# Kernel tuning notes

Measured on AMD Instinct MI355X. Metric: run time of the kernel, lower is better.

## Reference

```python
import jax, jax.numpy as jnp
import numpy as np

B, N, D = 256, 512, 512
H = 512            # step_context_dim
HEADS = 8
KEY = H // HEADS
T = 128            # number of decode steps
TANH_CLIP = 10.0
TEMP = 1.0
VEHICLE_CAP = 1.0
BATTERY_CAP = 1.0
NEG = -1e9         # stands in for -inf; safe under softmax/vjp


def setup_inputs() -> dict:
    key = jax.random.key(0)
    ks = jax.random.split(key, 10)
    embedding = jax.random.normal(ks[0], (B, N, D), dtype=jnp.float32)
    current_nodes = jax.random.randint(ks[1], (B, T), 0, N)
    used_capacity = jax.random.uniform(ks[2], (B, T), dtype=jnp.float32)
    used_battery = jax.random.uniform(ks[3], (B, T), dtype=jnp.float32)
    current_time = jax.random.uniform(ks[4], (B, T), dtype=jnp.float32)
    mask = jax.random.randint(ks[5], (B, T, N), 0, 2).astype(bool)
    mask = mask.at[:, :, 0].set(False)  # ensure at least one feasible node
    s = 0.02
    W_context = jax.random.normal(ks[6], (D, H), dtype=jnp.float32) * s
    W_kvlogit = jax.random.normal(ks[7], (D, 3 * H), dtype=jnp.float32) * s
    W_step = jax.random.normal(ks[8], (D + 3, H), dtype=jnp.float32) * s
    W_out = jax.random.normal(ks[9], (H, H), dtype=jnp.float32) * s
    return {"embedding": embedding, "current_nodes": current_nodes,
            "used_capacity": used_capacity, "used_battery": used_battery,
            "current_time": current_time, "mask": mask,
            "W_context": W_context, "W_kvlogit": W_kvlogit,
            "W_step": W_step, "W_out": W_out}


def reference(embedding, current_nodes, used_capacity, used_battery,
              current_time, mask, W_context, W_kvlogit, W_step, W_out):
    b, n, d = embedding.shape
    t = current_nodes.shape[1]
    # fixed context from mean graph embedding: [B,1,H]
    fixed_context = jnp.einsum('bd,dh->bh', embedding.mean(axis=1), W_context)[:, None, :]
    # shared K/V/logit-K projections: [B,N,3H]
    kvl = jnp.einsum('bnd,de->bne', embedding, W_kvlogit)
    glimpse_K, glimpse_V, logit_K = jnp.split(kvl, 3, axis=-1)
    glimpse_K = glimpse_K.reshape(b, n, HEADS, KEY).transpose(0, 2, 1, 3)  # [B,h,N,k]
    glimpse_V = glimpse_V.reshape(b, n, HEADS, KEY).transpose(0, 2, 1, 3)  # [B,h,N,k]
    # per-step context: gathered current-node embedding + 3 scalar state features
    cur_emb = jnp.take_along_axis(
        embedding, current_nodes[:, :, None], axis=1)  # [B,T,D]
    next_nodes = jnp.concatenate(
        [cur_emb,
         (VEHICLE_CAP - used_capacity)[..., None],
         (BATTERY_CAP - used_battery)[..., None],
         current_time[..., None]], axis=-1)            # [B,T,D+3]
    query = fixed_context + jnp.einsum('btd,dh->bth', next_nodes, W_step)  # [B,T,H]
    # multi-head single-query glimpse attention over all T steps at once
    Q = query.reshape(b, t, HEADS, KEY)
    compat = jnp.einsum('bthk,bhnk->bhtn', Q, glimpse_K) / np.sqrt(KEY)
    compat = jnp.where(mask[:, None, :, :], NEG, compat)
    attn = jax.nn.softmax(compat, axis=-1)
    heads_out = jnp.einsum('bhtn,bhnk->bthk', attn, glimpse_V).reshape(b, t, H)
    glimpse = jnp.einsum('bth,ho->bto', heads_out, W_out)  # project_out
    logits = jnp.einsum('bth,bnh->btn', glimpse, logit_K) / np.sqrt(H)
    logits = jnp.tanh(logits) * TANH_CLIP
    logits = jnp.where(mask, NEG, logits)
    log_p = jax.nn.log_softmax(logits / TEMP, axis=-1)  # [B,T,N]
    return log_p
```

## Files before the change

kernel.cpp:

```cpp
#include <hip/hip_runtime.h>
#include <hip/hip_bf16.h>
#include <hip/hip_fp8.h>
#include <stdint.h>

typedef unsigned char  u8;
typedef unsigned short u16;
typedef unsigned int   u32;
typedef unsigned long long u64;
typedef __attribute__((ext_vector_type(4))) float f32x4;
typedef __attribute__((ext_vector_type(8))) short s16x8;

#define NEG_INF (-1e9f)

__device__ __forceinline__ u16 f2bf(float f) {
  __hip_bfloat16 h = __float2bfloat16(f);
  return __builtin_bit_cast(u16, h);
}

__device__ __forceinline__ u8 f2fp8(float f) {
  __hip_fp8_e4m3 h(f);
  return (u8)h.__x;
}

__device__ __forceinline__ f32x4 mfma16(s16x8 a, s16x8 b, f32x4 c) {
  return __builtin_amdgcn_mfma_f32_16x16x32_bf16(a, b, c, 0, 0, 0);
}

__device__ __forceinline__ f32x4 mfma8(long a, long b, f32x4 c) {
  return __builtin_amdgcn_mfma_f32_16x16x32_fp8_fp8(a, b, c, 0, 0, 0);
}

#define GLOAD16(g, l)                                                        \
  __builtin_amdgcn_global_load_lds(                                          \
      (const __attribute__((address_space(1))) unsigned int*)(g),            \
      (__attribute__((address_space(3))) unsigned int*)(l), 16, 0, 0)
#define GLOAD4(g, l)                                                         \
  __builtin_amdgcn_global_load_lds(                                          \
      (const __attribute__((address_space(1))) unsigned int*)(g),            \
      (__attribute__((address_space(3))) unsigned int*)(l), 4, 0, 0)

#define WAITV(n) asm volatile("s_waitcnt vmcnt(" #n ")" ::: "memory")
#define WAITLGKM asm volatile("s_waitcnt lgkmcnt(0)" ::: "memory")
#define SBAR __builtin_amdgcn_sched_barrier(0)
#define HBAR __builtin_amdgcn_s_barrier()

__global__ void detect_mask_kernel(const u32* __restrict__ mraw, u32* __restrict__ flag) {
  __shared__ int any;
  if (threadIdx.x == 0) any = 0;
  __syncthreads();
  int loc = 0;
  for (int i = threadIdx.x; i < 16384; i += 256) {
    u32 v = mraw[i];
    if (v & 0xFFFFFF00u) loc = 1;
  }
  if (loc) atomicOr(&any, 1);
  __syncthreads();
  if (threadIdx.x == 0) *flag = any ? 1u : 4u;
}

__global__ __launch_bounds__(256) void maskprep_kernel(const void* __restrict__ mraw,
                                                       const u32* __restrict__ flag,
                                                       unsigned char* __restrict__ mb) {
  long long idx = (long long)blockIdx.x * 256 + threadIdx.x;
  long long bt = idx >> 6;
  int ch = (int)(idx & 63);
  unsigned char byte = 0;
  if (*flag == 1) {
    u64 v = *(const u64*)((const unsigned char*)mraw + bt * 512 + ch * 8);
#pragma unroll
    for (int i = 0; i < 8; i++)
      if ((v >> (8 * i)) & 0xFFull) byte |= (unsigned char)(1 << i);
  } else {
    const int* p = (const int*)mraw + bt * 512 + ch * 8;
#pragma unroll
    for (int i = 0; i < 8; i++)
      if (p[i]) byte |= (unsigned char)(1 << i);
  }
  mb[idx] = byte;
}

__global__ void transpose_cvt_kernel(const float* __restrict__ in, int ld_in, int off,
                                     int kreal, int CO, u16* __restrict__ outp) {
  int i = blockIdx.x;
  for (int j = threadIdx.x; j < CO; j += 256) {
    float v = (j < kreal) ? in[(long long)j * ld_in + off + i] : 0.0f;
    outp[(long long)i * CO + j] = f2bf(v);
  }
}

__global__ void transpose_cvt8_kernel(const float* __restrict__ in, u8* __restrict__ outp) {
  int i = blockIdx.x;
  for (int j = threadIdx.x; j < 512; j += 256)
    outp[(long long)i * 512 + j] = f2fp8(in[(long long)j * 1536 + i] * 16.0f);
}

__global__ void slice_cvt_kernel(const float* __restrict__ in, u16* __restrict__ outp) {
  long long idx = (long long)blockIdx.x * 256 + threadIdx.x;
  long long dd = idx >> 9;
  int hh = (int)(idx & 511);
  outp[idx] = f2bf(in[dd * 1536 + 1024 + hh]);
}

__global__ void cvt_bf_kernel(const float* __restrict__ in, u16* __restrict__ outp) {
  long long idx = (long long)blockIdx.x * 256 + threadIdx.x;
  outp[idx] = f2bf(in[idx]);
}

__global__ __launch_bounds__(256) void cvt_pmean_kernel(const float* __restrict__ emb,
                                                        u8* __restrict__ e8,
                                                        float* __restrict__ pmean) {
  const int bq = blockIdx.x >> 2, nq = blockIdx.x & 3;
  const int tid = threadIdx.x;
  const int ro = tid >> 7;
  const int c4 = (tid & 127) << 2;
  const long long base = ((long long)bq * 512 + nq * 128) * 512;
  float s[4] = {0.f, 0.f, 0.f, 0.f};
  for (int n = ro; n < 128; n += 2) {
    f32x4 v = *(const f32x4*)&emb[base + (long long)n * 512 + c4];
    u32 p8 = 0;
#pragma unroll
    for (int i = 0; i < 4; i++) {
      s[i] += v[i];
      p8 |= (u32)f2fp8(v[i]) << (8 * i);
    }
    *(u32*)&e8[base + (long long)n * 512 + c4] = p8;
  }
  __shared__ float ls[2][512];
#pragma unroll
  for (int i = 0; i < 4; i++) ls[ro][c4 + i] = s[i];
  __syncthreads();
  float* dst = pmean + (long long)blockIdx.x * 512;
  dst[tid] = ls[0][tid] + ls[1][tid];
  dst[tid + 256] = ls[0][tid + 256] + ls[1][tid + 256];
}

__global__ __launch_bounds__(256) void fixedctx_kernel(const float* __restrict__ pmean,
                                                       const float* __restrict__ Wc,
                                                       float* __restrict__ fixedc) {
  __shared__ float mf[512];
  int b = blockIdx.x;
  const float* p = pmean + (long long)b * 4 * 512;
  for (int d = threadIdx.x; d < 512; d += 256)
    mf[d] = (p[d] + p[512 + d] + p[1024 + d] + p[1536 + d]) * (1.0f / 512.0f);
  __syncthreads();
  for (int h = threadIdx.x; h < 512; h += 256) {
    float s = 0.f;
    for (int d = 0; d < 512; ++d) s += mf[d] * Wc[(long long)d * 512 + h];
    fixedc[(long long)b * 512 + h] = s;
  }
}

__global__ __launch_bounds__(256) void build_nextn_kernel(
    const float* __restrict__ emb, const int* __restrict__ cur,
    const float* __restrict__ ucap, const float* __restrict__ ubat,
    const float* __restrict__ ctim, u16* __restrict__ outp) {
  const long long rowm = (long long)blockIdx.x * 4 + (threadIdx.x >> 6);
  const int lane = threadIdx.x & 63;
  const int b = (int)(rowm >> 7);
  const int node = cur[rowm];
  const float* src = emb + ((long long)b * 512 + node) * 512;
  u16* dst = outp + rowm * 576;
  f32x4 a = *(const f32x4*)&src[lane * 8];
  f32x4 c = *(const f32x4*)&src[lane * 8 + 4];
  s16x8 pk;
#pragma unroll
  for (int i = 0; i < 4; i++) { pk[i] = (short)f2bf(a[i]); pk[i + 4] = (short)f2bf(c[i]); }
  *(s16x8*)&dst[lane * 8] = pk;
  {
    const int cc = 512 + lane;
    float v = (lane == 0) ? 1.0f - ucap[rowm]
            : (lane == 1) ? 1.0f - ubat[rowm]
            : (lane == 2) ? ctim[rowm] : 0.0f;
    dst[cc] = f2bf(v);
  }
}

__global__ __launch_bounds__(512, 4) void gemm_kv8_kernel(
    const u8* __restrict__ A8, const u8* __restrict__ Bw8,
    u8* __restrict__ K8, u8* __restrict__ V8) {
  __shared__ __align__(16) char lds[49152];
  const int tid = threadIdx.x;
  const int lane = tid & 63;
  const int wid = tid >> 6;
  const int wr = wid >> 1, wc = wid & 1;
  const int fr = lane & 15;
  const int fq = lane >> 4;

  const int p = blockIdx.x;
  const int x = p & 7;
  const int i = p >> 3;
  const int ntile = i & 7;
  const int mgrp = i >> 3;
  const long long nrow0 = (long long)ntile * 128;

  const int srow = tid >> 2;
  const int sc = tid & 3;

#define MROW(tt2) (((long long)x * 64 + mgrp * 8 + ((tt2) >> 3)) * 256)
#define KOF(tt2) (((tt2) & 7) * 64)

#define STAGEA(dd, tt2)                                                       \
  {                                                                           \
    _Pragma("unroll") for (int g_ = 0; g_ < 2; g_++) {                        \
      const int r_ = g_ * 128 + srow;                                         \
      GLOAD16(A8 + (MROW(tt2) + r_) * 512ll + KOF(tt2) +                      \
                  ((sc ^ ((r_ >> 1) & 3)) << 4),                              \
              lds + (dd) * 24576 + g_ * 8192 + wid * 1024);                   \
    }                                                                         \
  }
#define STAGEB(dd, tt2)                                                       \
  {                                                                           \
    GLOAD16(Bw8 + (nrow0 + srow) * 512ll + KOF(tt2) +                         \
                ((sc ^ ((srow >> 1) & 3)) << 4),                              \
            lds + (dd) * 24576 + 16384 + wid * 1024);                         \
  }

#define READ_A(dst, mb)                                                       \
  _Pragma("unroll") for (int ks = 0; ks < 2; ks++) {                          \
    const int r_ = wr * 64 + (mb) * 16 + fr;                                  \
    dst[ks] = *(const long*)(ab + r_ * 64 + (((ks * 4 + fq) ^ (r_ & 6)) << 3)); \
  }
#define MFMA_PH(src, mb)                                                      \
  _Pragma("unroll") for (int nb = 0; nb < 4; nb++)                            \
  _Pragma("unroll") for (int ks = 0; ks < 2; ks++)                            \
    acc[mb][nb] = mfma8(src[ks], bfrag[nb][ks], acc[mb][nb]);

  STAGEB(0, 0); STAGEA(0, 0);
  STAGEB(1, 1); STAGEA(1, 1);

  f32x4 acc[4][4];

#pragma unroll 1
  for (int u = 0; u < 8; u++) {
#pragma unroll
    for (int ii = 0; ii < 4; ii++)
#pragma unroll
      for (int jj = 0; jj < 4; jj++) acc[ii][jj] = (f32x4){0.f, 0.f, 0.f, 0.f};

#pragma unroll 1
    for (int t8 = 0; t8 < 8; t8++) {
      const int tt = u * 8 + t8;
      const int d = tt & 1;
      if (tt == 63) { WAITV(0); } else { WAITV(3); }
      HBAR; SBAR;

      const char* ab = lds + d * 24576;
      const char* bb = lds + d * 24576 + 16384;

      long bfrag[4][2];
#pragma unroll
      for (int nb = 0; nb < 4; nb++)
#pragma unroll
        for (int ks = 0; ks < 2; ks++) {
          const int brow = wc * 64 + nb * 16 + fr;
          bfrag[nb][ks] =
              *(const long*)(bb + brow * 64 + (((ks * 4 + fq) ^ (brow & 6)) << 3));
        }
      long afA[2], afB[2];
      READ_A(afA, 0);
      WAITLGKM; SBAR;
      READ_A(afB, 1);
      __builtin_amdgcn_s_setprio(1);
      MFMA_PH(afA, 0);
      __builtin_amdgcn_s_setprio(0);
      WAITLGKM; SBAR;
      READ_A(afA, 2);
      __builtin_amdgcn_s_setprio(1);
      MFMA_PH(afB, 1);
      __builtin_amdgcn_s_setprio(0);
      WAITLGKM; SBAR;
      READ_A(afB, 3);
      __builtin_amdgcn_s_setprio(1);
      MFMA_PH(afA, 2);
      __builtin_amdgcn_s_setprio(0);
      WAITLGKM; SBAR;
      HBAR;
      if (tt + 2 < 64) { STAGEB(d, tt + 2); STAGEA(d, tt + 2); }
      __builtin_amdgcn_s_setprio(1);
      MFMA_PH(afB, 3);
      __builtin_amdgcn_s_setprio(0);
    }

    const long long mrow0 = MROW(u * 8);
    const int colbase = (int)(ntile * 128) + wc * 64;
#pragma unroll
    for (int mb = 0; mb < 4; mb++) {
      const long long row = mrow0 + wr * 64 + mb * 16 + fq * 4;
      const int bbx = (int)(row >> 9);
      const int node0 = (int)(row & 511);
#pragma unroll
      for (int nb = 0; nb < 4; nb++) {
        const int col = colbase + nb * 16 + fr;
        const int hh = (col >> 6) & 7;
        const int kk = col & 63;
        if (col < 512) {
          u8* dst = K8 + (((long long)(bbx * 8 + hh) * 512 + node0) << 6) + kk;
#pragma unroll
          for (int q = 0; q < 4; q++)
            dst[(long long)q << 6] = f2fp8(acc[mb][nb][q] * 0.0625f);
        } else {
          u32 pw = 0;
#pragma unroll
          for (int q = 0; q < 4; q++)
            pw |= (u32)f2fp8(acc[mb][nb][q] * 0.0625f) << (8 * q);
          *(u32*)(V8 + (((long long)(bbx * 8 + hh) * 64 + kk) << 9) + node0) = pw;
        }
      }
    }
  }
#undef STAGEA
#undef STAGEB
#undef READ_A
#undef MFMA_PH
#undef MROW
#undef KOF
}

template <int MODE>
__global__ __launch_bounds__(512, 1) void gemmW_kernel(
    const u16* __restrict__ A, const u16* __restrict__ Bv,
    int ldA, int ldB, int NT,
    void* __restrict__ out0, const void* __restrict__ aux) {
  __shared__ __align__(16) char lds[98304];
  const int tid = threadIdx.x;
  const int lane = tid & 63;
  const int wid = tid >> 6;
  const int wr = wid >> 1, wc = wid & 1;

  const int p = blockIdx.x;
  const int chunk = (int)(gridDim.x >> 3);
  const int wk = (p & 7) * chunk + (p >> 3);
  const int mtile = wk >> 2;
  const int ntile = wk & 3;
  const long long mrow0 = (long long)mtile * 256;
  const u16* Bb = Bv + (long long)ntile * 128 * ldB;

  const int rsub = tid >> 3;
  const int ssl = tid & 7;

#define STAGEA(dd, k0)                                                        \
  {                                                                           \
    _Pragma("unroll") for (int g_ = 0; g_ < 4; g_++) {                        \
      const int r_ = g_ * 64 + rsub;                                          \
      const int colel_ = (k0) + ((ssl ^ (r_ & 7)) << 3);                      \
      GLOAD16(A + (mrow0 + r_) * (long long)ldA + colel_,                     \
              lds + (dd) * 32768 + g_ * 8192 + wid * 1024);                   \
    }                                                                         \
  }
#define STAGEB(dd, k0)                                                        \
  {                                                                           \
    _Pragma("unroll") for (int g_ = 0; g_ < 2; g_++) {                        \
      const int r_ = g_ * 64 + rsub;                                          \
      const int colel_ = (k0) + ((ssl ^ (r_ & 7)) << 3);                      \
      GLOAD16(Bb + r_ * (long long)ldB + colel_,                              \
              lds + 65536 + (dd) * 16384 + g_ * 8192 + wid * 1024);           \
    }                                                                         \
  }
#define READ_A1(dst, ph)                                                      \
  _Pragma("unroll") for (int ks = 0; ks < 2; ks++) {                          \
    const int arow = (ph) * 16 + fr;                                          \
    dst[ks] = *(const s16x8*)(ab + arow * 128 + ((ks * 64 + fq * 16) ^ swz)); \
  }
#define MFMA_P(src, ph)                                                       \
  _Pragma("unroll") for (int nb = 0; nb < 4; nb++)                            \
  _Pragma("unroll") for (int ks = 0; ks < 2; ks++)                            \
    acc[ph][nb] = mfma16(src[ks], bfrag[nb][ks], acc[ph][nb]);

  f32x4 acc[4][4];
#pragma unroll
  for (int ii = 0; ii < 4; ii++)
#pragma unroll
    for (int jj = 0; jj < 4; jj++) acc[ii][jj] = (f32x4){0.f, 0.f, 0.f, 0.f};

  STAGEB(0, 0); STAGEA(0, 0);
  STAGEB(1, 64); STAGEA(1, 64);

  const int fr = lane & 15;
  const int fq = lane >> 4;
  const int swz = (lane & 7) << 4;

#pragma unroll 1
  for (int t = 0; t < NT; t++) {
    const int d = t & 1;
    if (t == NT - 1) { WAITV(0); } else { WAITV(6); }
    HBAR; SBAR;

    const char* ab = lds + d * 32768 + wr * 8192;
    const char* bb = lds + 65536 + d * 16384 + wc * 8192;

    s16x8 bfrag[4][2];
#pragma unroll
    for (int nb = 0; nb < 4; nb++)
#pragma unroll
      for (int ks = 0; ks < 2; ks++) {
        const int brow = nb * 16 + fr;
        bfrag[nb][ks] =
            *(const s16x8*)(bb + brow * 128 + ((ks * 64 + fq * 16) ^ swz));
      }
    s16x8 afA[2], afB[2];
    READ_A1(afA, 0);
    WAITLGKM; SBAR;
    READ_A1(afB, 1);
    __builtin_amdgcn_s_setprio(1);
    MFMA_P(afA, 0);
    __builtin_amdgcn_s_setprio(0);
    WAITLGKM; SBAR;
    READ_A1(afA, 2);
    __builtin_amdgcn_s_setprio(1);
    MFMA_P(afB, 1);
    __builtin_amdgcn_s_setprio(0);
    WAITLGKM; SBAR;
    READ_A1(afB, 3);
    __builtin_amdgcn_s_setprio(1);
    MFMA_P(afA, 2);
    __builtin_amdgcn_s_setprio(0);
    WAITLGKM; SBAR;
    HBAR;
    if (t + 2 < NT) { STAGEB(d, (t + 2) * 64); STAGEA(d, (t + 2) * 64); }
    __builtin_amdgcn_s_setprio(1);
    MFMA_P(afB, 3);
    __builtin_amdgcn_s_setprio(0);
  }
#undef STAGEA
#undef STAGEB
#undef READ_A1
#undef MFMA_P

  const int colbase = ntile * 128 + wc * 64;
#pragma unroll
  for (int mb = 0; mb < 4; mb++) {
    const long long row0 = mrow0 + wr * 64 + mb * 16 + fq * 4;
#pragma unroll
    for (int nb = 0; nb < 4; nb++) {
      const int col = colbase + nb * 16 + fr;
#pragma unroll
      for (int q = 0; q < 4; q++) {
        const long long row = row0 + q;
        float v = acc[mb][nb][q];
        if (MODE == 2) {
          ((u8*)out0)[row * 512 + col] = f2fp8(v * 8.0f);
        } else {
          if (MODE == 0) {
            const float* fc = (const float*)aux;
            v += fc[(row >> 7) * 512 + col];
          }
          ((u16*)out0)[row * 512 + col] = f2bf(v);
        }
      }
    }
  }
}

__global__ __launch_bounds__(512, 4) void gemm_lsm8_kernel(
    const u8* __restrict__ e8, const u8* __restrict__ tmp8,
    const u64* __restrict__ maskb, float* __restrict__ outp) {
  __shared__ __align__(16) char lds[73728];
  const int tid = threadIdx.x;
  const int lane = tid & 63;
  const int wid = tid >> 6;
  const int fr = lane & 15;
  const int fq = lane >> 4;

  const int p = blockIdx.x;
  const int x = p & 7;
  const int i = p >> 3;
  const int thalf = i & 1;
  const int b = x * 32 + (i >> 1);

  const u8* Ab = e8 + (long long)b * 262144;
  const u8* Bb = tmp8 + (long long)b * 65536 + (long long)thalf * 64 * 512;

  const int srow = tid >> 2;
  const int sc = tid & 3;

#define STAGEA(dd, k0)                                                        \
  {                                                                           \
    _Pragma("unroll") for (int g_ = 0; g_ < 4; g_++) {                        \
      const int r_ = g_ * 128 + srow;                                         \
      GLOAD16(Ab + r_ * 512ll + (k0) + ((sc ^ ((r_ >> 1) & 3)) << 4),         \
              lds + (dd) * 32768 + g_ * 8192 + wid * 1024);                   \
    }                                                                         \
  }
#define STAGEB(dd, k0)                                                        \
  {                                                                           \
    _Pragma("unroll") for (int g_ = 0; g_ < 2; g_++) {                        \
      const int r_ = g_ * 32 + (tid >> 4);                                    \
      const int lb_ = (tid & 15) * 4;                                         \
      const int gb_ = ((((lb_ >> 4) ^ ((r_ >> 1) & 3))) << 4) | (lb_ & 15);   \
      GLOAD4(Bb + r_ * 512ll + (k0) + gb_,                                    \
             lds + 65536 + (dd) * 4096 + g_ * 2048 + wid * 256);              \
    }                                                                         \
  }
#define READ_A(dst, mb)                                                       \
  _Pragma("unroll") for (int ks = 0; ks < 2; ks++) {                          \
    const int r_ = wid * 64 + (mb) * 16 + fr;                                 \
    dst[ks] = *(const long*)(ab + r_ * 64 + (((ks * 4 + fq) ^ (r_ & 6)) << 3)); \
  }
#define MFMA_PH(src, mb)                                                      \
  _Pragma("unroll") for (int nb = 0; nb < 4; nb++)                            \
  _Pragma("unroll") for (int ks = 0; ks < 2; ks++)                            \
    acc[mb][nb] = mfma8(src[ks], bfrag[nb][ks], acc[mb][nb]);

  f32x4 acc[4][4];
#pragma unroll
  for (int ii = 0; ii < 4; ii++)
#pragma unroll
    for (int jj = 0; jj < 4; jj++) acc[ii][jj] = (f32x4){0.f, 0.f, 0.f, 0.f};

  STAGEB(0, 0); STAGEA(0, 0);
  STAGEB(1, 64); STAGEA(1, 64);

#pragma unroll 1
  for (int t = 0; t < 8; t++) {
    const int d = t & 1;
    if (t == 7) { WAITV(0); } else { WAITV(6); }
    HBAR; SBAR;

    const char* ab = lds + d * 32768;
    const char* bb = lds + 65536 + d * 4096;

    long bfrag[4][2];
#pragma unroll
    for (int nb = 0; nb < 4; nb++)
#pragma unroll
      for (int ks = 0; ks < 2; ks++) {
        const int brow = nb * 16 + fr;
        bfrag[nb][ks] =
            *(const long*)(bb + brow * 64 + (((ks * 4 + fq) ^ (brow & 6)) << 3));
      }
    long afA[2], afB[2];
    READ_A(afA, 0);
    WAITLGKM; SBAR;
    READ_A(afB, 1);
    __builtin_amdgcn_s_setprio(1);
    MFMA_PH(afA, 0);
    __builtin_amdgcn_s_setprio(0);
    WAITLGKM; SBAR;
    READ_A(afA, 2);
    __builtin_amdgcn_s_setprio(1);
    MFMA_PH(afB, 1);
    __builtin_amdgcn_s_setprio(0);
    WAITLGKM; SBAR;
    READ_A(afB, 3);
    __builtin_amdgcn_s_setprio(1);
    MFMA_PH(afA, 2);
    __builtin_amdgcn_s_setprio(0);
    WAITLGKM; SBAR;
    HBAR;
    if (t + 2 < 8) { STAGEB(d, (t + 2) * 64); STAGEA(d, (t + 2) * 64); }
    __builtin_amdgcn_s_setprio(1);
    MFMA_PH(afB, 3);
    __builtin_amdgcn_s_setprio(0);
  }
#undef STAGEA
#undef STAGEB
#undef READ_A
#undef MFMA_PH

  float* red = (float*)lds;
  const float rs8 = 0.044194173824159216f * 0.125f;
  const float L2E = 1.4426950408889634f;

  float lmax[4];
#pragma unroll
  for (int nb = 0; nb < 4; nb++) {
    const int tl = nb * 16 + fr;
    const long long orow = (long long)b * 128 + thalf * 64 + tl;
    const u64 w = maskb[orow * 8 + wid];
    float mx = -3.0e38f;
#pragma unroll
    for (int mb = 0; mb < 4; mb++) {
      f32x4 r;
#pragma unroll
      for (int q = 0; q < 4; q++) {
        float xv = acc[mb][nb][q] * rs8;
        float e = exp2f(xv * 2.8853900817779268f);
        float th = 1.0f - 2.0f * __builtin_amdgcn_rcpf(e + 1.0f);
        float lg = 10.0f * th;
        const int bitn = mb * 16 + fq * 4 + q;
        if ((w >> bitn) & 1ull) lg = NEG_INF;
        r[q] = lg;
        mx = fmaxf(mx, lg);
      }
      acc[mb][nb] = r;
    }
    mx = fmaxf(mx, __shfl_xor(mx, 16));
    mx = fmaxf(mx, __shfl_xor(mx, 32));
    lmax[nb] = mx;
  }
  __syncthreads();
  if (lane < 16) {
#pragma unroll
    for (int nb = 0; nb < 4; nb++) red[wid * 64 + nb * 16 + lane] = lmax[nb];
  }
  __syncthreads();
  if (tid < 64) {
    float m = red[tid];
#pragma unroll
    for (int ww = 1; ww < 8; ww++) m = fmaxf(m, red[ww * 64 + tid]);
    red[512 + tid] = m;
  }
  __syncthreads();
  float lsum[4];
#pragma unroll
  for (int nb = 0; nb < 4; nb++) {
    const float m = red[512 + nb * 16 + fr];
    float s = 0.f;
#pragma unroll
    for (int mb = 0; mb < 4; mb++)
#pragma unroll
      for (int q = 0; q < 4; q++) s += exp2f((acc[mb][nb][q] - m) * L2E);
    s += __shfl_xor(s, 16);
    s += __shfl_xor(s, 32);
    lsum[nb] = s;
  }
  if (lane < 16) {
#pragma unroll
    for (int nb = 0; nb < 4; nb++) red[576 + wid * 64 + nb * 16 + lane] = lsum[nb];
  }
  __syncthreads();
  if (tid < 64) {
    float s = red[576 + tid];
#pragma unroll
    for (int ww = 1; ww < 8; ww++) s += red[576 + ww * 64 + tid];
    red[1088 + tid] = red[512 + tid] + logf(s);
  }
  __syncthreads();
#pragma unroll
  for (int nb = 0; nb < 4; nb++) {
    const int tl = nb * 16 + fr;
    const long long orow = (long long)b * 128 + thalf * 64 + tl;
    const float lse = red[1088 + tl];
#pragma unroll
    for (int mb = 0; mb < 4; mb++) {
      const int node0 = wid * 64 + mb * 16 + fq * 4;
      f32x4 r = acc[mb][nb];
#pragma unroll
      for (int q = 0; q < 4; q++) r[q] -= lse;
      *(f32x4*)&outp[orow * 512 + node0] = r;
    }
  }
}

__global__ __launch_bounds__(256) void gemm128_plain_kernel(
    const u16* __restrict__ A, const u16* __restrict__ Bv, u16* __restrict__ outp) {
  __shared__ u16 lA[128 * 32];
  __shared__ u16 lB[128 * 32];
  const int tid = threadIdx.x;
  const int lane = tid & 63;
  const int wave = tid >> 6;
  const int wr = wave >> 1, wc = wave & 1;

  const int p = blockIdx.x;
  const int wk = (p & 7) * 2 + (p >> 3);
  const int ntile = wk & 3;
  const int mtile = wk >> 2;
  const long long arow0 = (long long)mtile * 128;
  const long long brow0 = (long long)ntile * 128;

  f32x4 acc[4][4];
#pragma unroll
  for (int i = 0; i < 4; i++)
#pragma unroll
    for (int j = 0; j < 4; j++) acc[i][j] = (f32x4){0.f, 0.f, 0.f, 0.f};

  const int sc8 = (lane & 3) << 3;

  for (int k0 = 0; k0 < 512; k0 += 32) {
    __syncthreads();
#pragma unroll
    for (int i = 0; i < 2; i++) {
      GLOAD16(A + (arow0 + i * 64 + wave * 16 + (lane >> 2)) * 512ll + k0 + sc8,
              &lA[(i * 64 + wave * 16) * 32]);
      GLOAD16(Bv + (brow0 + i * 64 + wave * 16 + (lane >> 2)) * 512ll + k0 + sc8,
              &lB[(i * 64 + wave * 16) * 32]);
    }
    __syncthreads();
    s16x8 af[4], bfr[4];
#pragma unroll
    for (int i = 0; i < 4; i++)
      af[i] = *(const s16x8*)&lA[(wr * 64 + i * 16 + (lane & 15)) * 32 + ((lane >> 4) << 3)];
#pragma unroll
    for (int j = 0; j < 4; j++)
      bfr[j] = *(const s16x8*)&lB[(wc * 64 + j * 16 + (lane & 15)) * 32 + ((lane >> 4) << 3)];
#pragma unroll
    for (int i = 0; i < 4; i++)
#pragma unroll
      for (int j = 0; j < 4; j++) acc[i][j] = mfma16(af[i], bfr[j], acc[i][j]);
  }

#pragma unroll
  for (int i = 0; i < 4; i++) {
    const int rl = wr * 64 + i * 16 + ((lane >> 4) << 2);
#pragma unroll
    for (int j = 0; j < 4; j++) {
      const int cl = wc * 64 + j * 16 + (lane & 15);
#pragma unroll
      for (int q = 0; q < 4; q++)
        outp[(arow0 + rl + q) * 512 + brow0 + cl] = f2bf(acc[i][j][q]);
    }
  }
}

__global__ __launch_bounds__(512, 4) void attn_kernel(
    const u16* __restrict__ query, const u8* __restrict__ K8,
    const u8* __restrict__ V8, const u64* __restrict__ maskbits,
    u16* __restrict__ headsout) {
  __shared__ __align__(16) char lds[68864];
  char* Plds = lds + 32768;
  float* rsw = (float*)(lds + 66560);
  float* rst = (float*)(lds + 68608);

  const int p = blockIdx.x;
  const int fb = (p & 7) * 512 + (p >> 3);
  const int thalf = fb & 1;
  const int h = (fb >> 1) & 7;
  const int b = fb >> 4;
  const int bh = b * 8 + h;
  const int tid = threadIdx.x;
  const int lane = tid & 63;
  const int wid = tid >> 6;
  const int fr = lane & 15;
  const int fq = lane >> 4;
  const int tt0 = thalf * 64;

  {
    const u8* Vb = V8 + (long long)bh * 32768;
#pragma unroll
    for (int it = 0; it < 4; it++) {
      const int row = it * 16 + (tid >> 5);
      const int s16 = tid & 31;
      GLOAD16(Vb + row * 512 + ((s16 ^ (row & 7)) << 4), lds + row * 512);
    }
  }

  const u16* Qb = query + ((long long)(b * 128 + tt0)) * 512 + h * 64;
  long qf[4][2];
#pragma unroll
  for (int tf = 0; tf < 4; tf++)
#pragma unroll
    for (int ks = 0; ks < 2; ks++) {
      s16x8 qv = *(const s16x8*)(Qb + (long long)(tf * 16 + fr) * 512 + ks * 32 + fq * 8);
      u64 pk = 0;
#pragma unroll
      for (int e = 0; e < 8; e++) {
        __hip_bfloat16 hb = __builtin_bit_cast(__hip_bfloat16, (u16)qv[e]);
        pk |= (u64)f2fp8(__bfloat162float(hb)) << (8 * e);
      }
      qf[tf][ks] = (long)pk;
    }

  const int wstrip = wid * 64;
  const u8* Kb = K8 + ((long long)bh * 512 + wstrip) * 64;
  f32x4 s[4][4];
#pragma unroll
  for (int nf = 0; nf < 4; nf++)
#pragma unroll
    for (int tf = 0; tf < 4; tf++) s[nf][tf] = (f32x4){0.f, 0.f, 0.f, 0.f};
#pragma unroll
  for (int nf = 0; nf < 4; nf++) {
#pragma unroll
    for (int ks = 0; ks < 2; ks++) {
      long kf = *(const long*)(Kb + (long long)(nf * 16 + fr) * 64 + ks * 32 + fq * 8);
#pragma unroll
      for (int tf = 0; tf < 4; tf++) s[nf][tf] = mfma8(kf, qf[tf][ks], s[nf][tf]);
    }
  }

  const float CE = 0.18033688011112043f;
  u64 mq[4];
#pragma unroll
  for (int tf = 0; tf < 4; tf++)
    mq[tf] = maskbits[((long long)(b * 128) + tt0 + tf * 16 + fr) * 8 + wid];
  float psum[4] = {0.f, 0.f, 0.f, 0.f};
#pragma unroll
  for (int nf = 0; nf < 4; nf++) {
#pragma unroll
    for (int tf = 0; tf < 4; tf++) {
      u32 pw = 0;
#pragma unroll
      for (int q = 0; q < 4; q++) {
        const int bit = nf * 16 + fq * 4 + q;
        float pv = exp2f(s[nf][tf][q] * CE);
        if ((mq[tf] >> bit) & 1ull) pv = 0.0f;
        psum[tf] += pv;
        pw |= (u32)f2fp8(pv) << (8 * q);
      }
      const int t = tf * 16 + fr;
      const int o = wstrip + nf * 16 + fq * 4;
      const int s8 = o >> 3, lo = o & 7;
      *(u32*)(Plds + t * 528 + (((s8 ^ (t & 7)) << 3) | lo)) = pw;
    }
  }
#pragma unroll
  for (int tf = 0; tf < 4; tf++) {
    float v = psum[tf];
    v += __shfl_xor(v, 16);
    v += __shfl_xor(v, 32);
    if (lane < 16) rsw[(tf * 16 + lane) * 8 + wid] = v;
  }
  __syncthreads();

  if (tid < 64) {
    float sum = rsw[tid * 8];
#pragma unroll
    for (int ww = 1; ww < 8; ww++) sum += rsw[tid * 8 + ww];
    rst[tid] = __builtin_amdgcn_rcpf(sum);
  }

  const int kkh = wid & 1;
  const int tts = wid >> 1;
  f32x4 o[2];
  o[0] = (f32x4){0.f, 0.f, 0.f, 0.f};
  o[1] = (f32x4){0.f, 0.f, 0.f, 0.f};
  const int tpv = tts * 16 + fr;
#pragma unroll
  for (int nstep = 0; nstep < 16; nstep++) {
    const int s8 = nstep * 4 + fq;
    long pf = *(const long*)(Plds + tpv * 528 + ((s8 ^ (tpv & 7)) << 3));
#pragma unroll
    for (int kf = 0; kf < 2; kf++) {
      const int kk = kkh * 32 + kf * 16 + fr;
      const int vs16 = s8 >> 1, vlo = s8 & 1;
      long vf = *(const long*)(lds + kk * 512 + (((vs16 ^ (kk & 7)) << 4) | (vlo << 3)));
      o[kf] = mfma8(vf, pf, o[kf]);
    }
  }
  __syncthreads();

  const float r = rst[tpv];
  const long long orow = (long long)b * 128 + tt0 + tpv;
#pragma unroll
  for (int kf = 0; kf < 2; kf++) {
    u16 pk[4];
#pragma unroll
    for (int q = 0; q < 4; q++) pk[q] = f2bf(o[kf][q] * r);
    const int col = h * 64 + kkh * 32 + kf * 16 + fq * 4;
    *(u64*)&headsout[orow * 512 + col] =
        (u64)pk[0] | ((u64)pk[1] << 16) | ((u64)pk[2] << 32) | ((u64)pk[3] << 48);
  }
}

extern "C" void kernel_launch(void* const* d_in, const int* in_sizes, int n_in,
                              void* d_out, int out_size, void* d_ws, size_t ws_size,
                              hipStream_t stream) {
  (void)in_sizes; (void)n_in; (void)out_size; (void)ws_size;
  const float* emb  = (const float*)d_in[0];
  const int*   cur  = (const int*)d_in[1];
  const float* ucap = (const float*)d_in[2];
  const float* ubat = (const float*)d_in[3];
  const float* ctim = (const float*)d_in[4];
  const void*  mask = d_in[5];
  const float* Wc   = (const float*)d_in[6];
  const float* Wkvl = (const float*)d_in[7];
  const float* Wstep= (const float*)d_in[8];
  const float* Wout = (const float*)d_in[9];

  char* w = (char*)d_ws;
  size_t off = 0;
  auto take = [&](size_t nbytes) -> char* {
    char* p = w + off;
    off += (nbytes + 255) & ~(size_t)255;
    return p;
  };
  u32* flag            = (u32*)take(4);
  unsigned char* maskb = (unsigned char*)take((size_t)256 * 128 * 64);
  u8* e8               = (u8*)take((size_t)256 * 512 * 512);
  u8* WkT8             = (u8*)take((size_t)1024 * 512);
  u16* WstepT          = (u16*)take((size_t)512 * 576 * 2);
  u16* W2bf            = (u16*)take((size_t)512 * 512 * 2);
  u16* Woutbf          = (u16*)take((size_t)512 * 512 * 2);
  u16* WfT             = (u16*)take((size_t)512 * 512 * 2);
  float* pmean         = (float*)take((size_t)1024 * 512 * 4);
  float* fixedc        = (float*)take((size_t)256 * 512 * 4);
  u8* K8               = (u8*)take((size_t)256 * 8 * 512 * 64);
  u8* V8               = (u8*)take((size_t)256 * 8 * 64 * 512);
  u8* tmp8             = (u8*)take((size_t)32768 * 512);
  u16* slotA           = (u16*)take((size_t)32768 * 576 * 2);
  u16* slotB           = (u16*)take((size_t)32768 * 512 * 2);
  u16* nextn = slotA;
  u16* query = slotB;
  u16* headsout = slotA;

  detect_mask_kernel<<<1, 256, 0, stream>>>((const u32*)mask, flag);
  maskprep_kernel<<<8192, 256, 0, stream>>>(mask, flag, maskb);
  transpose_cvt8_kernel<<<1024, 256, 0, stream>>>(Wkvl, WkT8);
  transpose_cvt_kernel<<<512, 256, 0, stream>>>(Wstep, 512, 0, 515, 576, WstepT);
  slice_cvt_kernel<<<1024, 256, 0, stream>>>(Wkvl, W2bf);
  cvt_bf_kernel<<<1024, 256, 0, stream>>>(Wout, Woutbf);
  gemm128_plain_kernel<<<16, 256, 0, stream>>>(W2bf, Woutbf, WfT);
  cvt_pmean_kernel<<<1024, 256, 0, stream>>>(emb, e8, pmean);
  fixedctx_kernel<<<256, 256, 0, stream>>>(pmean, Wc, fixedc);
  build_nextn_kernel<<<8192, 256, 0, stream>>>(emb, cur, ucap, ubat, ctim, nextn);

  gemm_kv8_kernel<<<512, 512, 0, stream>>>(e8, WkT8, K8, V8);
  gemmW_kernel<0><<<512, 512, 0, stream>>>(nextn, WstepT, 576, 576, 9, query, fixedc);
  attn_kernel<<<4096, 512, 0, stream>>>(query, K8, V8, (const u64*)maskb, headsout);
  gemmW_kernel<2><<<512, 512, 0, stream>>>(headsout, WfT, 512, 512, 8, tmp8, nullptr);
  gemm_lsm8_kernel<<<512, 512, 0, stream>>>(e8, tmp8, (const u64*)maskb, (float*)d_out);
}
```

Baseline: 550.8 us.

## Move step-query and output-projection GEMMs and their intermediates to FP8

Switches the query projection and the head-output projection GEMMs from bf16 MFMA to fp8 MFMA, with fp8 weights and fp8 activations carrying fixed scale factors. The gathered node features now come from the existing fp8 embedding copy, and the attention kernel reads the fp8 query directly and writes fp8 head outputs. This halves the bytes moved between stages, allows more resident blocks through smaller LDS use, and removes the bf16 to fp8 conversion inside attention. In exchange it loses precision in the query and head outputs, including the small scalar state features that are now stored as fp8.

```diff
diff --git a/kernel.cpp b/kernel.cpp
--- a/kernel.cpp
+++ b/kernel.cpp
@@ -79,19 +79,13 @@
   mb[idx] = byte;
 }
 
-__global__ void transpose_cvt_kernel(const float* __restrict__ in, int ld_in, int off,
-                                     int kreal, int CO, u16* __restrict__ outp) {
+__global__ void tcvt8_kernel(const float* __restrict__ in, int ld_in, int kreal,
+                             int CO, u8* __restrict__ outp) {
   int i = blockIdx.x;
   for (int j = threadIdx.x; j < CO; j += 256) {
-    float v = (j < kreal) ? in[(long long)j * ld_in + off + i] : 0.0f;
-    outp[(long long)i * CO + j] = f2bf(v);
-  }
-}
-
-__global__ void transpose_cvt8_kernel(const float* __restrict__ in, u8* __restrict__ outp) {
-  int i = blockIdx.x;
-  for (int j = threadIdx.x; j < 512; j += 256)
-    outp[(long long)i * 512 + j] = f2fp8(in[(long long)j * 1536 + i] * 16.0f);
+    float v = (j < kreal) ? in[(long long)j * ld_in + i] * 16.0f : 0.0f;
+    outp[(long long)i * CO + j] = f2fp8(v);
+  }
 }
 
 __global__ void slice_cvt_kernel(const float* __restrict__ in, u16* __restrict__ outp) {
@@ -150,28 +144,24 @@
   }
 }
 
-__global__ __launch_bounds__(256) void build_nextn_kernel(
-    const float* __restrict__ emb, const int* __restrict__ cur,
+__global__ __launch_bounds__(256) void build_nextn8_kernel(
+    const u8* __restrict__ e8, const int* __restrict__ cur,
     const float* __restrict__ ucap, const float* __restrict__ ubat,
-    const float* __restrict__ ctim, u16* __restrict__ outp) {
+    const float* __restrict__ ctim, u8* __restrict__ outp) {
   const long long rowm = (long long)blockIdx.x * 4 + (threadIdx.x >> 6);
   const int lane = threadIdx.x & 63;
   const int b = (int)(rowm >> 7);
   const int node = cur[rowm];
-  const float* src = emb + ((long long)b * 512 + node) * 512;
-  u16* dst = outp + rowm * 576;
-  f32x4 a = *(const f32x4*)&src[lane * 8];
-  f32x4 c = *(const f32x4*)&src[lane * 8 + 4];
-  s16x8 pk;
-#pragma unroll
-  for (int i = 0; i < 4; i++) { pk[i] = (short)f2bf(a[i]); pk[i + 4] = (short)f2bf(c[i]); }
-  *(s16x8*)&dst[lane * 8] = pk;
-  {
-    const int cc = 512 + lane;
-    float v = (lane == 0) ? 1.0f - ucap[rowm]
-            : (lane == 1) ? 1.0f - ubat[rowm]
-            : (lane == 2) ? ctim[rowm] : 0.0f;
-    dst[cc] = f2bf(v);
+  const u8* src = e8 + ((long long)b * 512 + node) * 512;
+  u8* dst = outp + rowm * 576;
+  *(u64*)&dst[lane * 8] = *(const u64*)&src[lane * 8];
+  if (lane < 8) {
+    u64 v = 0;
+    if (lane == 0) {
+      v = (u64)f2fp8(1.0f - ucap[rowm]) | ((u64)f2fp8(1.0f - ubat[rowm]) << 8) |
+          ((u64)f2fp8(ctim[rowm]) << 16);
+    }
+    *(u64*)&dst[512 + lane * 8] = v;
   }
 }
 
@@ -317,54 +307,52 @@
 }
 
 template <int MODE>
-__global__ __launch_bounds__(512, 1) void gemmW_kernel(
-    const u16* __restrict__ A, const u16* __restrict__ Bv,
+__global__ __launch_bounds__(512, 4) void gemm8_kernel(
+    const u8* __restrict__ A8, const u8* __restrict__ B8,
     int ldA, int ldB, int NT,
-    void* __restrict__ out0, const void* __restrict__ aux) {
-  __shared__ __align__(16) char lds[98304];
+    u8* __restrict__ out0, const float* __restrict__ aux) {
+  __shared__ __align__(16) char lds[49152];
   const int tid = threadIdx.x;
   const int lane = tid & 63;
   const int wid = tid >> 6;
   const int wr = wid >> 1, wc = wid & 1;
+  const int fr = lane & 15;
+  const int fq = lane >> 4;
 
   const int p = blockIdx.x;
-  const int chunk = (int)(gridDim.x >> 3);
-  const int wk = (p & 7) * chunk + (p >> 3);
+  const int wk = (p & 7) * 64 + (p >> 3);
   const int mtile = wk >> 2;
   const int ntile = wk & 3;
   const long long mrow0 = (long long)mtile * 256;
-  const u16* Bb = Bv + (long long)ntile * 128 * ldB;
-
-  const int rsub = tid >> 3;
-  const int ssl = tid & 7;
-
-#define STAGEA(dd, k0)                                                        \
-  {                                                                           \
-    _Pragma("unroll") for (int g_ = 0; g_ < 4; g_++) {                        \
-      const int r_ = g_ * 64 + rsub;                                          \
-      const int colel_ = (k0) + ((ssl ^ (r_ & 7)) << 3);                      \
-      GLOAD16(A + (mrow0 + r_) * (long long)ldA + colel_,                     \
-              lds + (dd) * 32768 + g_ * 8192 + wid * 1024);                   \
-    }                                                                         \
-  }
-#define STAGEB(dd, k0)                                                        \
+  const long long nrow0 = (long long)ntile * 128;
+
+  const int srow = tid >> 2;
+  const int sc = tid & 3;
+
+#define STAGEA8(dd, k0)                                                       \
   {                                                                           \
     _Pragma("unroll") for (int g_ = 0; g_ < 2; g_++) {                        \
-      const int r_ = g_ * 64 + rsub;                                          \
-      const int colel_ = (k0) + ((ssl ^ (r_ & 7)) << 3);                      \
-      GLOAD16(Bb + r_ * (long long)ldB + colel_,                              \
-              lds + 65536 + (dd) * 16384 + g_ * 8192 + wid * 1024);           \
+      const int r_ = g_ * 128 + srow;                                         \
+      GLOAD16(A8 + (mrow0 + r_) * (long long)ldA + (k0) +                     \
+                  ((sc ^ ((r_ >> 1) & 3)) << 4),                              \
+              lds + (dd) * 24576 + g_ * 8192 + wid * 1024);                   \
     }                                                                         \
   }
-#define READ_A1(dst, ph)                                                      \
+#define STAGEB8(dd, k0)                                                       \
+  {                                                                           \
+    GLOAD16(B8 + (nrow0 + srow) * (long long)ldB + (k0) +                     \
+                ((sc ^ ((srow >> 1) & 3)) << 4),                              \
+            lds + (dd) * 24576 + 16384 + wid * 1024);                         \
+  }
+#define READ_A8(dst, mb)                                                      \
   _Pragma("unroll") for (int ks = 0; ks < 2; ks++) {                          \
-    const int arow = (ph) * 16 + fr;                                          \
-    dst[ks] = *(const s16x8*)(ab + arow * 128 + ((ks * 64 + fq * 16) ^ swz)); \
-  }
-#define MFMA_P(src, ph)                                                       \
+    const int r_ = wr * 64 + (mb) * 16 + fr;                                  \
+    dst[ks] = *(const long*)(ab + r_ * 64 + (((ks * 4 + fq) ^ (r_ & 6)) << 3)); \
+  }
+#define MFMA_PH8(src, mb)                                                     \
   _Pragma("unroll") for (int nb = 0; nb < 4; nb++)                            \
   _Pragma("unroll") for (int ks = 0; ks < 2; ks++)                            \
-    acc[ph][nb] = mfma16(src[ks], bfrag[nb][ks], acc[ph][nb]);
+    acc[mb][nb] = mfma8(src[ks], bfrag[nb][ks], acc[mb][nb]);
 
   f32x4 acc[4][4];
 #pragma unroll
@@ -372,61 +360,57 @@
 #pragma unroll
     for (int jj = 0; jj < 4; jj++) acc[ii][jj] = (f32x4){0.f, 0.f, 0.f, 0.f};
 
-  STAGEB(0, 0); STAGEA(0, 0);
-  STAGEB(1, 64); STAGEA(1, 64);
-
-  const int fr = lane & 15;
-  const int fq = lane >> 4;
-  const int swz = (lane & 7) << 4;
+  STAGEB8(0, 0); STAGEA8(0, 0);
+  STAGEB8(1, 64); STAGEA8(1, 64);
 
 #pragma unroll 1
   for (int t = 0; t < NT; t++) {
     const int d = t & 1;
-    if (t == NT - 1) { WAITV(0); } else { WAITV(6); }
+    if (t == NT - 1) { WAITV(0); } else { WAITV(3); }
     HBAR; SBAR;
 
-    const char* ab = lds + d * 32768 + wr * 8192;
-    const char* bb = lds + 65536 + d * 16384 + wc * 8192;
-
-    s16x8 bfrag[4][2];
+    const char* ab = lds + d * 24576;
+    const char* bb = lds + d * 24576 + 16384;
+
+    long bfrag[4][2];
 #pragma unroll
     for (int nb = 0; nb < 4; nb++)
 #pragma unroll
       for (int ks = 0; ks < 2; ks++) {
-        const int brow = nb * 16 + fr;
+        const int brow = wc * 64 + nb * 16 + fr;
         bfrag[nb][ks] =
-            *(const s16x8*)(bb + brow * 128 + ((ks * 64 + fq * 16) ^ swz));
+            *(const long*)(bb + brow * 64 + (((ks * 4 + fq) ^ (brow & 6)) << 3));
       }
-    s16x8 afA[2], afB[2];
-    READ_A1(afA, 0);
+    long afA[2], afB[2];
+    READ_A8(afA, 0);
     WAITLGKM; SBAR;
-    READ_A1(afB, 1);
+    READ_A8(afB, 1);
     __builtin_amdgcn_s_setprio(1);
-    MFMA_P(afA, 0);
+    MFMA_PH8(afA, 0);
     __builtin_amdgcn_s_setprio(0);
     WAITLGKM; SBAR;
-    READ_A1(afA, 2);
+    READ_A8(afA, 2);
     __builtin_amdgcn_s_setprio(1);
-    MFMA_P(afB, 1);
+    MFMA_PH8(afB, 1);
     __builtin_amdgcn_s_setprio(0);
     WAITLGKM; SBAR;
-    READ_A1(afB, 3);
+    READ_A8(afB, 3);
     __builtin_amdgcn_s_setprio(1);
-    MFMA_P(afA, 2);
+    MFMA_PH8(afA, 2);
     __builtin_amdgcn_s_setprio(0);
     WAITLGKM; SBAR;
     HBAR;
-    if (t + 2 < NT) { STAGEB(d, (t + 2) * 64); STAGEA(d, (t + 2) * 64); }
+    if (t + 2 < NT) { STAGEB8(d, (t + 2) * 64); STAGEA8(d, (t + 2) * 64); }
     __builtin_amdgcn_s_setprio(1);
-    MFMA_P(afB, 3);
+    MFMA_PH8(afB, 3);
     __builtin_amdgcn_s_setprio(0);
   }
-#undef STAGEA
-#undef STAGEB
-#undef READ_A1
-#undef MFMA_P
-
-  const int colbase = ntile * 128 + wc * 64;
+#undef STAGEA8
+#undef STAGEB8
+#undef READ_A8
+#undef MFMA_PH8
+
+  const int colbase = (int)(ntile * 128) + wc * 64;
 #pragma unroll
   for (int mb = 0; mb < 4; mb++) {
     const long long row0 = mrow0 + wr * 64 + mb * 16 + fq * 4;
@@ -436,15 +420,11 @@
 #pragma unroll
       for (int q = 0; q < 4; q++) {
         const long long row = row0 + q;
-        float v = acc[mb][nb][q];
-        if (MODE == 2) {
-          ((u8*)out0)[row * 512 + col] = f2fp8(v * 8.0f);
+        if (MODE == 0) {
+          float v = acc[mb][nb][q] * 0.0625f + aux[(row >> 7) * 512 + col];
+          out0[row * 512 + col] = f2fp8(v * 2.0f);
         } else {
-          if (MODE == 0) {
-            const float* fc = (const float*)aux;
-            v += fc[(row >> 7) * 512 + col];
-          }
-          ((u16*)out0)[row * 512 + col] = f2bf(v);
+          out0[row * 512 + col] = f2fp8(acc[mb][nb][q] * 0.03125f);
         }
       }
     }
@@ -643,7 +623,7 @@
 }
 
 __global__ __launch_bounds__(256) void gemm128_plain_kernel(
-    const u16* __restrict__ A, const u16* __restrict__ Bv, u16* __restrict__ outp) {
+    const u16* __restrict__ A, const u16* __restrict__ Bv, u8* __restrict__ outp) {
   __shared__ u16 lA[128 * 32];
   __shared__ u16 lB[128 * 32];
   const int tid = threadIdx.x;
@@ -697,15 +677,15 @@
       const int cl = wc * 64 + j * 16 + (lane & 15);
 #pragma unroll
       for (int q = 0; q < 4; q++)
-        outp[(arow0 + rl + q) * 512 + brow0 + cl] = f2bf(acc[i][j][q]);
+        outp[(arow0 + rl + q) * 512 + brow0 + cl] = f2fp8(acc[i][j][q] * 64.0f);
     }
   }
 }
 
 __global__ __launch_bounds__(512, 4) void attn_kernel(
-    const u16* __restrict__ query, const u8* __restrict__ K8,
+    const u8* __restrict__ q8, const u8* __restrict__ K8,
     const u8* __restrict__ V8, const u64* __restrict__ maskbits,
-    u16* __restrict__ headsout) {
+    u8* __restrict__ o8buf) {
   __shared__ __align__(16) char lds[68864];
   char* Plds = lds + 32768;
   float* rsw = (float*)(lds + 66560);
@@ -734,21 +714,13 @@
     }
   }
 
-  const u16* Qb = query + ((long long)(b * 128 + tt0)) * 512 + h * 64;
+  const u8* Qb = q8 + ((long long)(b * 128 + tt0)) * 512 + h * 64;
   long qf[4][2];
 #pragma unroll
   for (int tf = 0; tf < 4; tf++)
 #pragma unroll
-    for (int ks = 0; ks < 2; ks++) {
-      s16x8 qv = *(const s16x8*)(Qb + (long long)(tf * 16 + fr) * 512 + ks * 32 + fq * 8);
-      u64 pk = 0;
-#pragma unroll
-      for (int e = 0; e < 8; e++) {
-        __hip_bfloat16 hb = __builtin_bit_cast(__hip_bfloat16, (u16)qv[e]);
-        pk |= (u64)f2fp8(__bfloat162float(hb)) << (8 * e);
-      }
-      qf[tf][ks] = (long)pk;
-    }
+    for (int ks = 0; ks < 2; ks++)
+      qf[tf][ks] = *(const long*)(Qb + (long long)(tf * 16 + fr) * 512 + ks * 32 + fq * 8);
 
   const int wstrip = wid * 64;
   const u8* Kb = K8 + ((long long)bh * 512 + wstrip) * 64;
@@ -767,7 +739,7 @@
     }
   }
 
-  const float CE = 0.18033688011112043f;
+  const float CE2 = 0.09016844005556021f;
   u64 mq[4];
 #pragma unroll
   for (int tf = 0; tf < 4; tf++)
@@ -781,7 +753,7 @@
 #pragma unroll
       for (int q = 0; q < 4; q++) {
         const int bit = nf * 16 + fq * 4 + q;
-        float pv = exp2f(s[nf][tf][q] * CE);
+        float pv = exp2f(s[nf][tf][q] * CE2);
         if ((mq[tf] >> bit) & 1ull) pv = 0.0f;
         psum[tf] += pv;
         pw |= (u32)f2fp8(pv) << (8 * q);
@@ -828,16 +800,15 @@
   }
   __syncthreads();
 
-  const float r = rst[tpv];
+  const float r4 = rst[tpv] * 4.0f;
   const long long orow = (long long)b * 128 + tt0 + tpv;
 #pragma unroll
   for (int kf = 0; kf < 2; kf++) {
-    u16 pk[4];
-#pragma unroll
-    for (int q = 0; q < 4; q++) pk[q] = f2bf(o[kf][q] * r);
+    u32 pw = 0;
+#pragma unroll
+    for (int q = 0; q < 4; q++) pw |= (u32)f2fp8(o[kf][q] * r4) << (8 * q);
     const int col = h * 64 + kkh * 32 + kf * 16 + fq * 4;
-    *(u64*)&headsout[orow * 512 + col] =
-        (u64)pk[0] | ((u64)pk[1] << 16) | ((u64)pk[2] << 32) | ((u64)pk[3] << 48);
+    *(u32*)&o8buf[orow * 512 + col] = pw;
   }
 }
 
@@ -867,35 +838,33 @@
   unsigned char* maskb = (unsigned char*)take((size_t)256 * 128 * 64);
   u8* e8               = (u8*)take((size_t)256 * 512 * 512);
   u8* WkT8             = (u8*)take((size_t)1024 * 512);
-  u16* WstepT          = (u16*)take((size_t)512 * 576 * 2);
+  u8* WstepT8          = (u8*)take((size_t)512 * 576);
   u16* W2bf            = (u16*)take((size_t)512 * 512 * 2);
   u16* Woutbf          = (u16*)take((size_t)512 * 512 * 2);
-  u16* WfT             = (u16*)take((size_t)512 * 512 * 2);
+  u8* WfT8             = (u8*)take((size_t)512 * 512);
   float* pmean         = (float*)take((size_t)1024 * 512 * 4);
   float* fixedc        = (float*)take((size_t)256 * 512 * 4);
   u8* K8               = (u8*)take((size_t)256 * 8 * 512 * 64);
   u8* V8               = (u8*)take((size_t)256 * 8 * 64 * 512);
+  u8* nextn8           = (u8*)take((size_t)32768 * 576);
+  u8* q8               = (u8*)take((size_t)32768 * 512);
+  u8* o8               = (u8*)take((size_t)32768 * 512);
   u8* tmp8             = (u8*)take((size_t)32768 * 512);
-  u16* slotA           = (u16*)take((size_t)32768 * 576 * 2);
-  u16* slotB           = (u16*)take((size_t)32768 * 512 * 2);
-  u16* nextn = slotA;
-  u16* query = slotB;
-  u16* headsout = slotA;
 
   detect_mask_kernel<<<1, 256, 0, stream>>>((const u32*)mask, flag);
   maskprep_kernel<<<8192, 256, 0, stream>>>(mask, flag, maskb);
-  transpose_cvt8_kernel<<<1024, 256, 0, stream>>>(Wkvl, WkT8);
-  transpose_cvt_kernel<<<512, 256, 0, stream>>>(Wstep, 512, 0, 515, 576, WstepT);
+  tcvt8_kernel<<<1024, 256, 0, stream>>>(Wkvl, 1536, 512, 512, WkT8);
+  tcvt8_kernel<<<512, 256, 0, stream>>>(Wstep, 512, 515, 576, WstepT8);
   slice_cvt_kernel<<<1024, 256, 0, stream>>>(Wkvl, W2bf);
   cvt_bf_kernel<<<1024, 256, 0, stream>>>(Wout, Woutbf);
-  gemm128_plain_kernel<<<16, 256, 0, stream>>>(W2bf, Woutbf, WfT);
+  gemm128_plain_kernel<<<16, 256, 0, stream>>>(W2bf, Woutbf, WfT8);
   cvt_pmean_kernel<<<1024, 256, 0, stream>>>(emb, e8, pmean);
   fixedctx_kernel<<<256, 256, 0, stream>>>(pmean, Wc, fixedc);
-  build_nextn_kernel<<<8192, 256, 0, stream>>>(emb, cur, ucap, ubat, ctim, nextn);
+  build_nextn8_kernel<<<8192, 256, 0, stream>>>(e8, cur, ucap, ubat, ctim, nextn8);
 
   gemm_kv8_kernel<<<512, 512, 0, stream>>>(e8, WkT8, K8, V8);
-  gemmW_kernel<0><<<512, 512, 0, stream>>>(nextn, WstepT, 576, 576, 9, query, fixedc);
-  attn_kernel<<<4096, 512, 0, stream>>>(query, K8, V8, (const u64*)maskb, headsout);
-  gemmW_kernel<2><<<512, 512, 0, stream>>>(headsout, WfT, 512, 512, 8, tmp8, nullptr);
+  gemm8_kernel<0><<<512, 512, 0, stream>>>(nextn8, WstepT8, 576, 576, 9, q8, fixedc);
+  attn_kernel<<<4096, 512, 0, stream>>>(q8, K8, V8, (const u64*)maskb, o8);
+  gemm8_kernel<1><<<512, 512, 0, stream>>>(o8, WfT8, 512, 512, 8, tmp8, nullptr);
   gemm_lsm8_kernel<<<512, 512, 0, stream>>>(e8, tmp8, (const u64*)maskb, (float*)d_out);
 }
```

Result: faster. 510.7 us (-7.3%).
